# Kernel tuning notes

Hardware: AMD Instinct MI355X
Metric: run time of the kernel (lower is better)

Reference implementation:

```python
import jax, jax.numpy as jnp
import numpy as np

HIDDEN = 4096
INTER = 11008
BATCH, SEQ = 2, 2048


def setup_inputs() -> dict:
    key = jax.random.key(0)
    ks = jax.random.split(key, 7)
    s_h = 1.0 / np.sqrt(HIDDEN)   # nn.Linear default init bound fan_in=HIDDEN
    s_i = 1.0 / np.sqrt(INTER)    # fan_in=INTER for down_proj
    return {
        "hidden_states": jax.random.normal(ks[0], (BATCH, SEQ, HIDDEN), dtype=jnp.float32),
        "w_gate": jax.random.uniform(ks[1], (INTER, HIDDEN), jnp.float32, -s_h, s_h),
        "b_gate": jax.random.uniform(ks[2], (INTER,), jnp.float32, -s_h, s_h),
        "w_up": jax.random.uniform(ks[3], (INTER, HIDDEN), jnp.float32, -s_h, s_h),
        "b_up": jax.random.uniform(ks[4], (INTER,), jnp.float32, -s_h, s_h),
        "w_down": jax.random.uniform(ks[5], (HIDDEN, INTER), jnp.float32, -s_i, s_i),
        "b_down": jax.random.uniform(ks[6], (HIDDEN,), jnp.float32, -s_i, s_i),
    }


def reference(hidden_states, w_gate, b_gate, w_up, b_up, w_down, b_down):
    # SwiGLU MLP: down( silu(gate(x)) * up(x) )
    gate = jax.nn.silu(jnp.einsum("bsh,ih->bsi", hidden_states, w_gate) + b_gate)
    up = jnp.einsum("bsh,ih->bsi", hidden_states, w_up) + b_up
    return jnp.einsum("bsi,hi->bsh", gate * up, w_down) + b_down
```

## Files before the change

kernel.cpp:

```cpp
#include <hip/hip_runtime.h>
#include <hip/hip_bf16.h>


#define M_TOK 4096
#define HID   4096
#define INT_  11008

typedef __attribute__((ext_vector_type(8))) short bf16x8;
typedef __attribute__((ext_vector_type(4))) float f32x4;

__device__ __forceinline__ unsigned short f2bf(float f) {
    union { float f; unsigned int u; } a; a.f = f;
    unsigned int u = a.u;
    u += 0x7fff + ((u >> 16) & 1);
    return (unsigned short)(u >> 16);
}

__device__ __forceinline__ float bf2f(unsigned short h) {
    union { unsigned int u; float f; } a; a.u = ((unsigned int)h) << 16;
    return a.f;
}

__global__ void cvt_f32_bf16(const float* __restrict__ in, unsigned short* __restrict__ out, int n4) {
    int stride = gridDim.x * blockDim.x;
    for (int i = blockIdx.x * blockDim.x + threadIdx.x; i < n4; i += stride) {
        float4 v = ((const float4*)in)[i];
        ushort4 o;
        o.x = f2bf(v.x); o.y = f2bf(v.y); o.z = f2bf(v.z); o.w = f2bf(v.w);
        ((ushort4*)out)[i] = o;
    }
}

#define GLL(gsrc, ldst) \
    __builtin_amdgcn_global_load_lds( \
        (__attribute__((address_space(1))) void*)(gsrc), \
        (__attribute__((address_space(3))) void*)(ldst), 16, 0, 0)

#define VMC(n) asm volatile("s_waitcnt vmcnt(" #n ")" ::: "memory")
#define BARR __builtin_amdgcn_s_barrier()
#define PIN  __builtin_amdgcn_sched_barrier(0)

__global__ __launch_bounds__(512, 2)
void gemm_gu(const unsigned short* __restrict__ A,
             const unsigned short* __restrict__ Wg,
             const unsigned short* __restrict__ Wu,
             const float* __restrict__ bg,
             const float* __restrict__ bu,
             unsigned short* __restrict__ T,
             int M, int NI, int K) {
    __shared__ unsigned short lds[2 * 32768];

    const int tid  = threadIdx.x;
    const int lane = tid & 63;
    const int w    = tid >> 6;
    const int wm   = w >> 2;
    const int wn   = w & 3;

    const int ntn = NI >> 7;
    const int chunk = gridDim.x >> 3;
    const int sw = (blockIdx.x & 7) * chunk + (blockIdx.x >> 3);
    const int bm = sw / ntn, bn = sw % ntn;

    const unsigned short* Ag  = A  + (size_t)(bm * 256) * K;
    const unsigned short* Bgg = Wg + (size_t)(bn * 128) * K;
    const unsigned short* Bug = Wu + (size_t)(bn * 128) * K;

    int offA[2][2], offBW[2];
#pragma unroll
    for (int i = 0; i < 2; ++i) {
        int sig = i * 512 + tid;
        int r   = sig >> 3;
        int s   = (sig & 7) ^ (r & 7);
#pragma unroll
        for (int h = 0; h < 2; ++h) {
            int grow = ((r >> 6) * 2 + h) * 64 + (r & 63);
            offA[h][i] = grow * K + s * 8;
        }
        offBW[i] = r * K + s * 8;
    }

    const int rl = lane & 15;
    const int kg = lane >> 4;
    const int x  = rl & 7;
    const int aRow  = (wm * 64 + rl) * 64;
    const int bGoff = 16384 + (wn * 32 + rl) * 64;
    const int bUoff = 24576 + (wn * 32 + rl) * 64;
    int slt[2];
#pragma unroll
    for (int ks = 0; ks < 2; ++ks) slt[ks] = ((ks * 4 + kg) ^ x) * 8;

    f32x4 accg[2][8], accu[2][8];
#pragma unroll
    for (int q = 0; q < 2; ++q)
#pragma unroll
        for (int f = 0; f < 8; ++f) {
            accg[q][f] = (f32x4){0.f, 0.f, 0.f, 0.f};
            accu[q][f] = (f32x4){0.f, 0.f, 0.f, 0.f};
        }

    const int NT = K >> 6;

#define STAGE_A(H, DST, SRC) \
    GLL((SRC) + offA[H][0], (DST) + (H) * 8192 + tid * 8); \
    GLL((SRC) + offA[H][1], (DST) + (H) * 8192 + 4096 + tid * 8)
#define STAGE_W(BASE, DST, SRC) \
    GLL((SRC) + offBW[0], (DST) + (BASE) + tid * 8); \
    GLL((SRC) + offBW[1], (DST) + (BASE) + 4096 + tid * 8)

#define RD_A(BUF, QM, DST) \
    { _Pragma("unroll") for (int ks = 0; ks < 2; ++ks) \
      _Pragma("unroll") for (int fm = 0; fm < 4; ++fm) \
        DST[ks * 4 + fm] = *(const bf16x8*)((BUF) + (QM) * 8192 + aRow + fm * 1024 + slt[ks]); }
#define RD_W(BUF, ROFF, DST) \
    { _Pragma("unroll") for (int ks = 0; ks < 2; ++ks) \
      _Pragma("unroll") for (int fn = 0; fn < 2; ++fn) \
        DST[ks * 2 + fn] = *(const bf16x8*)((BUF) + (ROFF) + fn * 1024 + slt[ks]); }
#define Q16(ACC, QM, AF, BF) \
    { _Pragma("unroll") for (int ks = 0; ks < 2; ++ks) \
      _Pragma("unroll") for (int fm = 0; fm < 4; ++fm) \
      _Pragma("unroll") for (int fn = 0; fn < 2; ++fn) \
        ACC[QM][fm * 2 + fn] = __builtin_amdgcn_mfma_f32_16x16x32_bf16( \
            AF[ks * 4 + fm], BF[ks * 2 + fn], ACC[QM][fm * 2 + fn], 0, 0, 0); }

    bf16x8 A0f[8], A1f[8], Bgf[4], Buf_[4];

    STAGE_A(0, lds, Ag);
    STAGE_W(16384, lds, Bgg);
    STAGE_W(24576, lds, Bug);
    STAGE_A(1, lds, Ag);
    VMC(2);
    BARR; PIN;

    for (int t = 0; t < NT; ++t) {
        const unsigned short* bc = lds + (t & 1) * 32768;
        unsigned short* sb = lds + ((t + 1) & 1) * 32768;
        const int ts = (t + 1 < NT) ? (t + 1) : (NT - 1);
        const unsigned short* sA = Ag + (size_t)ts * 64;
        const unsigned short* sG = Bgg + (size_t)ts * 64;
        const unsigned short* sU = Bug + (size_t)ts * 64;

        RD_A(bc, 0, A0f);
        RD_W(bc, bGoff, Bgf);
        STAGE_A(0, sb, sA);
        Q16(accg, 0, A0f, Bgf);
        RD_W(bc, bUoff, Buf_);
        STAGE_W(16384, sb, sG);
        Q16(accu, 0, A0f, Buf_);
        STAGE_W(24576, sb, sU);
        VMC(6);
        BARR; PIN;

        RD_A(bc, 1, A1f);
        STAGE_A(1, sb, sA);
        Q16(accg, 1, A1f, Bgf);
        Q16(accu, 1, A1f, Buf_);
        VMC(2);
        BARR; PIN;
    }
#undef RD_A
#undef RD_W
#undef Q16
#undef STAGE_A
#undef STAGE_W

    const int rbase = bm * 256 + wm * 128 + (lane >> 4) * 4;
    const int cbase = bn * 128 + wn * 32 + (lane & 15);
#pragma unroll
    for (int qm = 0; qm < 2; ++qm)
#pragma unroll
        for (int fn = 0; fn < 2; ++fn) {
            const int col = cbase + fn * 16;
            const float bgv = bg[col];
            const float buv = bu[col];
#pragma unroll
            for (int fm = 0; fm < 4; ++fm) {
                const int rb = rbase + qm * 64 + fm * 16;
#pragma unroll
                for (int j = 0; j < 4; ++j) {
                    float g = accg[qm][fm * 2 + fn][j] + bgv;
                    float u = accu[qm][fm * 2 + fn][j] + buv;
                    float s = g / (1.f + __expf(-g)) * u;
                    T[(size_t)(rb + j) * (size_t)INT_ + col] = f2bf(s);
                }
            }
        }
}

__global__ __launch_bounds__(512, 2)
void gemm_dn(const unsigned short* __restrict__ A,
             const unsigned short* __restrict__ B,
             const float* __restrict__ bias,
             float* __restrict__ C,
             int M, int N, int K) {
    __shared__ unsigned short lds[2 * 32768];

    const int tid  = threadIdx.x;
    const int lane = tid & 63;
    const int w    = tid >> 6;
    const int wm   = w >> 2;
    const int wn   = w & 3;

    const int ntn = N >> 8;
    const int chunk = gridDim.x >> 3;
    const int sw = (blockIdx.x & 7) * chunk + (blockIdx.x >> 3);
    const int bm = sw / ntn, bn = sw % ntn;

    const unsigned short* Ag = A + (size_t)(bm * 256) * K;
    const unsigned short* Bg = B + (size_t)(bn * 256) * K;

    int offA[2][2], offB[2][2];
#pragma unroll
    for (int h = 0; h < 2; ++h)
#pragma unroll
        for (int i = 0; i < 2; ++i) {
            int sig = i * 512 + tid;
            int r   = sig >> 3;
            int s   = (sig & 7) ^ (r & 7);
            int grow = ((r >> 6) * 2 + h) * 64 + (r & 63);
            int gcol = ((r >> 5) * 2 + h) * 32 + (r & 31);
            offA[h][i] = grow * K + s * 8;
            offB[h][i] = gcol * K + s * 8;
        }

    const int rl = lane & 15;
    const int kg = lane >> 4;
    const int x  = rl & 7;
    const int aRow = (wm * 64 + rl) * 64;
    const int bRow = 16384 + (wn * 32 + rl) * 64;
    int slt[2];
#pragma unroll
    for (int ks = 0; ks < 2; ++ks) slt[ks] = ((ks * 4 + kg) ^ x) * 8;

    f32x4 acc[2][2][8];
#pragma unroll
    for (int qm = 0; qm < 2; ++qm)
#pragma unroll
        for (int qn = 0; qn < 2; ++qn)
#pragma unroll
            for (int f = 0; f < 8; ++f)
                acc[qm][qn][f] = (f32x4){0.f, 0.f, 0.f, 0.f};

    const int NT = K >> 6;

#define STAGE_A(H, DST, SRC) \
    GLL((SRC) + offA[H][0], (DST) + (H) * 8192 + tid * 8); \
    GLL((SRC) + offA[H][1], (DST) + (H) * 8192 + 4096 + tid * 8)
#define STAGE_B(H, DST, SRC) \
    GLL((SRC) + offB[H][0], (DST) + 16384 + (H) * 8192 + tid * 8); \
    GLL((SRC) + offB[H][1], (DST) + 16384 + (H) * 8192 + 4096 + tid * 8)
#define RD_A(BUF, QM, DST) \
    { _Pragma("unroll") for (int ks = 0; ks < 2; ++ks) \
      _Pragma("unroll") for (int fm = 0; fm < 4; ++fm) \
        DST[ks * 4 + fm] = *(const bf16x8*)((BUF) + (QM) * 8192 + aRow + fm * 1024 + slt[ks]); }
#define RD_B(BUF, QN, DST) \
    { _Pragma("unroll") for (int ks = 0; ks < 2; ++ks) \
      _Pragma("unroll") for (int fn = 0; fn < 2; ++fn) \
        DST[ks * 2 + fn] = *(const bf16x8*)((BUF) + (QN) * 8192 + bRow + fn * 1024 + slt[ks]); }
#define Q16(QM, QN, AF, BF) \
    { _Pragma("unroll") for (int ks = 0; ks < 2; ++ks) \
      _Pragma("unroll") for (int fm = 0; fm < 4; ++fm) \
      _Pragma("unroll") for (int fn = 0; fn < 2; ++fn) \
        acc[QM][QN][fm * 2 + fn] = __builtin_amdgcn_mfma_f32_16x16x32_bf16( \
            AF[ks * 4 + fm], BF[ks * 2 + fn], acc[QM][QN][fm * 2 + fn], 0, 0, 0); }

    bf16x8 A0f[8], A1f[8], B0f[4], B1f[4];

    STAGE_A(0, lds, Ag); STAGE_B(0, lds, Bg); STAGE_B(1, lds, Bg); STAGE_A(1, lds, Ag);
    VMC(2);
    BARR; PIN;

    for (int t = 0; t < NT; ++t) {
        const unsigned short* bc = lds + (t & 1) * 32768;
        unsigned short* sb = lds + ((t + 1) & 1) * 32768;
        const int ts = (t + 1 < NT) ? (t + 1) : (NT - 1);
        const unsigned short* sAt = Ag + (size_t)ts * 64;
        const unsigned short* sBt = Bg + (size_t)ts * 64;

        RD_A(bc, 0, A0f);
        RD_B(bc, 0, B0f);
        STAGE_A(0, sb, sAt);
        Q16(0, 0, A0f, B0f);
        RD_B(bc, 1, B1f);
        STAGE_B(0, sb, sBt);
        Q16(0, 1, A0f, B1f);
        STAGE_B(1, sb, sBt);
        VMC(6);
        BARR; PIN;

        RD_A(bc, 1, A1f);
        STAGE_A(1, sb, sAt);
        Q16(1, 1, A1f, B1f);
        Q16(1, 0, A1f, B0f);
        VMC(2);
        BARR; PIN;
    }
#undef RD_A
#undef RD_B
#undef Q16
#undef STAGE_A
#undef STAGE_B

    const int rbase = bm * 256 + wm * 128 + (lane >> 4) * 4;
    const int cbase = bn * 256 + wn * 64 + (lane & 15);
#pragma unroll
    for (int qm = 0; qm < 2; ++qm)
#pragma unroll
        for (int qn = 0; qn < 2; ++qn)
#pragma unroll
            for (int fn = 0; fn < 2; ++fn) {
                const int col = cbase + qn * 32 + fn * 16;
                const float bv = bias[col];
#pragma unroll
                for (int fm = 0; fm < 4; ++fm) {
                    const int rb = rbase + qm * 64 + fm * 16;
#pragma unroll
                    for (int j = 0; j < 4; ++j)
                        C[(size_t)(rb + j) * (size_t)N + col] = acc[qm][qn][fm * 2 + fn][j] + bv;
                }
            }
}

extern "C" void kernel_launch(void* const* d_in, const int* in_sizes, int n_in,
                              void* d_out, int out_size, void* d_ws, size_t ws_size,
                              hipStream_t stream) {
    const float* x  = (const float*)d_in[0];
    const float* wg = (const float*)d_in[1];
    const float* bg = (const float*)d_in[2];
    const float* wu = (const float*)d_in[3];
    const float* bu = (const float*)d_in[4];
    const float* wd = (const float*)d_in[5];
    const float* bd = (const float*)d_in[6];

    const size_t NX = (size_t)M_TOK * HID;
    const size_t NW = (size_t)INT_ * HID;

    unsigned short* ws = (unsigned short*)d_ws;
    unsigned short* Xb = ws;
    unsigned short* S1 = Xb + NX;
    unsigned short* S2 = S1 + NW;
    unsigned short* S3 = S2 + NW;

    dim3 blk512(512);
    dim3 blk256(256);
    const int CG = 2048;

    cvt_f32_bf16<<<CG, blk256, 0, stream>>>(x,  Xb, (int)(NX / 4));
    cvt_f32_bf16<<<CG, blk256, 0, stream>>>(wg, S1, (int)(NW / 4));
    cvt_f32_bf16<<<CG, blk256, 0, stream>>>(wu, S2, (int)(NW / 4));
    gemm_gu<<<dim3(16 * 86), blk512, 0, stream>>>(Xb, S1, S2, bg, bu, S3,
                                                  M_TOK, INT_, HID);
    cvt_f32_bf16<<<CG, blk256, 0, stream>>>(wd, S1, (int)(NW / 4));
    gemm_dn<<<dim3(16 * 16), blk512, 0, stream>>>(S3, S1, bd, (float*)d_out,
                                                  M_TOK, HID, INT_);
}
```

Baseline: 1.013 ms.

## Fuse fp32-to-bf16 weight conversion into GEMM tile staging via registers

Removes the three separate weight conversion kernels and has both GEMMs read fp32 weights directly from global memory into registers, convert them to bf16 and write them into LDS. This avoids writing and re-reading bf16 copies of roughly 135M weight elements per call. In exchange, every M-tile block re-reads the weights at twice the byte width, uses more registers and VGPR-to-LDS writes instead of direct global-to-LDS loads, and adds extra waitcnt synchronisation to the pipeline.

```diff
diff --git a/kernel.cpp b/kernel.cpp
--- a/kernel.cpp
+++ b/kernel.cpp
@@ -16,9 +16,13 @@
     return (unsigned short)(u >> 16);
 }
 
-__device__ __forceinline__ float bf2f(unsigned short h) {
-    union { unsigned int u; float f; } a; a.u = ((unsigned int)h) << 16;
-    return a.f;
+__device__ __forceinline__ bf16x8 pack8(f32x4 a, f32x4 b) {
+    bf16x8 r;
+    r[0] = (short)f2bf(a[0]); r[1] = (short)f2bf(a[1]);
+    r[2] = (short)f2bf(a[2]); r[3] = (short)f2bf(a[3]);
+    r[4] = (short)f2bf(b[0]); r[5] = (short)f2bf(b[1]);
+    r[6] = (short)f2bf(b[2]); r[7] = (short)f2bf(b[3]);
+    return r;
 }
 
 __global__ void cvt_f32_bf16(const float* __restrict__ in, unsigned short* __restrict__ out, int n4) {
@@ -37,13 +41,24 @@
         (__attribute__((address_space(3))) void*)(ldst), 16, 0, 0)
 
 #define VMC(n) asm volatile("s_waitcnt vmcnt(" #n ")" ::: "memory")
+#define LGKM0  asm volatile("s_waitcnt lgkmcnt(0)" ::: "memory")
 #define BARR __builtin_amdgcn_s_barrier()
 #define PIN  __builtin_amdgcn_sched_barrier(0)
 
+#define WLOAD(DST, SRC, O0, O1) \
+    DST[0] = *(const f32x4*)((SRC) + (O0));      \
+    DST[1] = *(const f32x4*)((SRC) + (O0) + 4);  \
+    DST[2] = *(const f32x4*)((SRC) + (O1));      \
+    DST[3] = *(const f32x4*)((SRC) + (O1) + 4);
+
+#define WWRITE(BASE, SBUF, REGS) \
+    *(bf16x8*)((SBUF) + (BASE) + tid * 8)        = pack8(REGS[0], REGS[1]); \
+    *(bf16x8*)((SBUF) + (BASE) + 4096 + tid * 8) = pack8(REGS[2], REGS[3]);
+
 __global__ __launch_bounds__(512, 2)
 void gemm_gu(const unsigned short* __restrict__ A,
-             const unsigned short* __restrict__ Wg,
-             const unsigned short* __restrict__ Wu,
+             const float* __restrict__ Wg,
+             const float* __restrict__ Wu,
              const float* __restrict__ bg,
              const float* __restrict__ bu,
              unsigned short* __restrict__ T,
@@ -62,10 +77,10 @@
     const int bm = sw / ntn, bn = sw % ntn;
 
     const unsigned short* Ag  = A  + (size_t)(bm * 256) * K;
-    const unsigned short* Bgg = Wg + (size_t)(bn * 128) * K;
-    const unsigned short* Bug = Wu + (size_t)(bn * 128) * K;
-
-    int offA[2][2], offBW[2];
+    const float* Wgg = Wg + (size_t)(bn * 128) * K;
+    const float* Wug = Wu + (size_t)(bn * 128) * K;
+
+    int offA[2][2], offW[2];
 #pragma unroll
     for (int i = 0; i < 2; ++i) {
         int sig = i * 512 + tid;
@@ -76,7 +91,7 @@
             int grow = ((r >> 6) * 2 + h) * 64 + (r & 63);
             offA[h][i] = grow * K + s * 8;
         }
-        offBW[i] = r * K + s * 8;
+        offW[i] = r * K + s * 8;
     }
 
     const int rl = lane & 15;
@@ -103,10 +118,6 @@
 #define STAGE_A(H, DST, SRC) \
     GLL((SRC) + offA[H][0], (DST) + (H) * 8192 + tid * 8); \
     GLL((SRC) + offA[H][1], (DST) + (H) * 8192 + 4096 + tid * 8)
-#define STAGE_W(BASE, DST, SRC) \
-    GLL((SRC) + offBW[0], (DST) + (BASE) + tid * 8); \
-    GLL((SRC) + offBW[1], (DST) + (BASE) + 4096 + tid * 8)
-
 #define RD_A(BUF, QM, DST) \
     { _Pragma("unroll") for (int ks = 0; ks < 2; ++ks) \
       _Pragma("unroll") for (int fm = 0; fm < 4; ++fm) \
@@ -123,12 +134,17 @@
             AF[ks * 4 + fm], BF[ks * 2 + fn], ACC[QM][fm * 2 + fn], 0, 0, 0); }
 
     bf16x8 A0f[8], A1f[8], Bgf[4], Buf_[4];
-
+    f32x4 wgr[4], wur[4];
+
+    WLOAD(wgr, Wgg, offW[0], offW[1]);
+    WLOAD(wur, Wug, offW[0], offW[1]);
+    PIN;
     STAGE_A(0, lds, Ag);
-    STAGE_W(16384, lds, Bgg);
-    STAGE_W(24576, lds, Bug);
     STAGE_A(1, lds, Ag);
-    VMC(2);
+    WWRITE(16384, lds, wgr);
+    WWRITE(24576, lds, wur);
+    VMC(0);
+    LGKM0;
     BARR; PIN;
 
     for (int t = 0; t < NT; ++t) {
@@ -136,32 +152,36 @@
         unsigned short* sb = lds + ((t + 1) & 1) * 32768;
         const int ts = (t + 1 < NT) ? (t + 1) : (NT - 1);
         const unsigned short* sA = Ag + (size_t)ts * 64;
-        const unsigned short* sG = Bgg + (size_t)ts * 64;
-        const unsigned short* sU = Bug + (size_t)ts * 64;
+        const float* sG = Wgg + (size_t)ts * 64;
+        const float* sU = Wug + (size_t)ts * 64;
 
         RD_A(bc, 0, A0f);
         RD_W(bc, bGoff, Bgf);
+        RD_W(bc, bUoff, Buf_);
+        WLOAD(wgr, sG, offW[0], offW[1]);
+        WLOAD(wur, sU, offW[0], offW[1]);
+        PIN;
         STAGE_A(0, sb, sA);
         Q16(accg, 0, A0f, Bgf);
-        RD_W(bc, bUoff, Buf_);
-        STAGE_W(16384, sb, sG);
         Q16(accu, 0, A0f, Buf_);
-        STAGE_W(24576, sb, sU);
-        VMC(6);
+        VMC(10);
         BARR; PIN;
 
         RD_A(bc, 1, A1f);
         STAGE_A(1, sb, sA);
         Q16(accg, 1, A1f, Bgf);
         Q16(accu, 1, A1f, Buf_);
+        VMC(4);
+        WWRITE(16384, sb, wgr);
+        WWRITE(24576, sb, wur);
         VMC(2);
+        LGKM0;
         BARR; PIN;
     }
 #undef RD_A
 #undef RD_W
 #undef Q16
 #undef STAGE_A
-#undef STAGE_W
 
     const int rbase = bm * 256 + wm * 128 + (lane >> 4) * 4;
     const int cbase = bn * 128 + wn * 32 + (lane & 15);
@@ -188,7 +208,7 @@
 
 __global__ __launch_bounds__(512, 2)
 void gemm_dn(const unsigned short* __restrict__ A,
-             const unsigned short* __restrict__ B,
+             const float* __restrict__ B,
              const float* __restrict__ bias,
              float* __restrict__ C,
              int M, int N, int K) {
@@ -206,9 +226,9 @@
     const int bm = sw / ntn, bn = sw % ntn;
 
     const unsigned short* Ag = A + (size_t)(bm * 256) * K;
-    const unsigned short* Bg = B + (size_t)(bn * 256) * K;
-
-    int offA[2][2], offB[2][2];
+    const float* Bg = B + (size_t)(bn * 256) * K;
+
+    int offA[2][2], offW[2][2];
 #pragma unroll
     for (int h = 0; h < 2; ++h)
 #pragma unroll
@@ -219,7 +239,7 @@
             int grow = ((r >> 6) * 2 + h) * 64 + (r & 63);
             int gcol = ((r >> 5) * 2 + h) * 32 + (r & 31);
             offA[h][i] = grow * K + s * 8;
-            offB[h][i] = gcol * K + s * 8;
+            offW[h][i] = gcol * K + s * 8;
         }
 
     const int rl = lane & 15;
@@ -245,9 +265,6 @@
 #define STAGE_A(H, DST, SRC) \
     GLL((SRC) + offA[H][0], (DST) + (H) * 8192 + tid * 8); \
     GLL((SRC) + offA[H][1], (DST) + (H) * 8192 + 4096 + tid * 8)
-#define STAGE_B(H, DST, SRC) \
-    GLL((SRC) + offB[H][0], (DST) + 16384 + (H) * 8192 + tid * 8); \
-    GLL((SRC) + offB[H][1], (DST) + 16384 + (H) * 8192 + 4096 + tid * 8)
 #define RD_A(BUF, QM, DST) \
     { _Pragma("unroll") for (int ks = 0; ks < 2; ++ks) \
       _Pragma("unroll") for (int fm = 0; fm < 4; ++fm) \
@@ -264,9 +281,17 @@
             AF[ks * 4 + fm], BF[ks * 2 + fn], acc[QM][QN][fm * 2 + fn], 0, 0, 0); }
 
     bf16x8 A0f[8], A1f[8], B0f[4], B1f[4];
-
-    STAGE_A(0, lds, Ag); STAGE_B(0, lds, Bg); STAGE_B(1, lds, Bg); STAGE_A(1, lds, Ag);
-    VMC(2);
+    f32x4 w0[4], w1[4];
+
+    WLOAD(w0, Bg, offW[0][0], offW[0][1]);
+    WLOAD(w1, Bg, offW[1][0], offW[1][1]);
+    PIN;
+    STAGE_A(0, lds, Ag);
+    STAGE_A(1, lds, Ag);
+    WWRITE(16384, lds, w0);
+    WWRITE(24576, lds, w1);
+    VMC(0);
+    LGKM0;
     BARR; PIN;
 
     for (int t = 0; t < NT; ++t) {
@@ -274,31 +299,35 @@
         unsigned short* sb = lds + ((t + 1) & 1) * 32768;
         const int ts = (t + 1 < NT) ? (t + 1) : (NT - 1);
         const unsigned short* sAt = Ag + (size_t)ts * 64;
-        const unsigned short* sBt = Bg + (size_t)ts * 64;
+        const float* sBt = Bg + (size_t)ts * 64;
 
         RD_A(bc, 0, A0f);
         RD_B(bc, 0, B0f);
+        WLOAD(w0, sBt, offW[0][0], offW[0][1]);
+        WLOAD(w1, sBt, offW[1][0], offW[1][1]);
+        PIN;
         STAGE_A(0, sb, sAt);
         Q16(0, 0, A0f, B0f);
         RD_B(bc, 1, B1f);
-        STAGE_B(0, sb, sBt);
         Q16(0, 1, A0f, B1f);
-        STAGE_B(1, sb, sBt);
-        VMC(6);
+        VMC(10);
         BARR; PIN;
 
         RD_A(bc, 1, A1f);
         STAGE_A(1, sb, sAt);
         Q16(1, 1, A1f, B1f);
         Q16(1, 0, A1f, B0f);
+        VMC(4);
+        WWRITE(16384, sb, w0);
+        WWRITE(24576, sb, w1);
         VMC(2);
+        LGKM0;
         BARR; PIN;
     }
 #undef RD_A
 #undef RD_B
 #undef Q16
 #undef STAGE_A
-#undef STAGE_B
 
     const int rbase = bm * 256 + wm * 128 + (lane >> 4) * 4;
     const int cbase = bn * 256 + wn * 64 + (lane & 15);
@@ -332,24 +361,18 @@
     const float* bd = (const float*)d_in[6];
 
     const size_t NX = (size_t)M_TOK * HID;
-    const size_t NW = (size_t)INT_ * HID;
+    const size_t NW = (size_t)M_TOK * INT_;
 
     unsigned short* ws = (unsigned short*)d_ws;
     unsigned short* Xb = ws;
-    unsigned short* S1 = Xb + NX;
-    unsigned short* S2 = S1 + NW;
-    unsigned short* S3 = S2 + NW;
+    unsigned short* Tt = Xb + NX;
 
     dim3 blk512(512);
     dim3 blk256(256);
-    const int CG = 2048;
-
-    cvt_f32_bf16<<<CG, blk256, 0, stream>>>(x,  Xb, (int)(NX / 4));
-    cvt_f32_bf16<<<CG, blk256, 0, stream>>>(wg, S1, (int)(NW / 4));
-    cvt_f32_bf16<<<CG, blk256, 0, stream>>>(wu, S2, (int)(NW / 4));
-    gemm_gu<<<dim3(16 * 86), blk512, 0, stream>>>(Xb, S1, S2, bg, bu, S3,
+
+    cvt_f32_bf16<<<2048, blk256, 0, stream>>>(x, Xb, (int)(NX / 4));
+    gemm_gu<<<dim3(16 * 86), blk512, 0, stream>>>(Xb, wg, wu, bg, bu, Tt,
                                                   M_TOK, INT_, HID);
-    cvt_f32_bf16<<<CG, blk256, 0, stream>>>(wd, S1, (int)(NW / 4));
-    gemm_dn<<<dim3(16 * 16), blk512, 0, stream>>>(S3, S1, bd, (float*)d_out,
+    gemm_dn<<<dim3(16 * 16), blk512, 0, stream>>>(Tt, wd, bd, (float*)d_out,
                                                   M_TOK, HID, INT_);
 }
```

After: 1.557 ms. 1.54x slower.

## Merge input conversions into one kernel and overlap w_down conversion with gate/up GEMM

Applied to the files above, without the earlier changes.

The three fp32-to-bf16 conversion launches for x, w_gate and w_up become one kernel. The w_down conversion now runs as 128 extra blocks appended to the gate/up GEMM grid, writing into a fourth workspace buffer, so it can overlap with the GEMM tail instead of being a separate serialized launch. This path needs a larger workspace and falls back to the old sequence when the workspace is too small. The extra blocks compete with GEMM blocks for CUs and bandwidth.

```diff
diff --git a/kernel.cpp b/kernel.cpp
--- a/kernel.cpp
+++ b/kernel.cpp
@@ -5,6 +5,8 @@
 #define M_TOK 4096
 #define HID   4096
 #define INT_  11008
+#define NGU   1376
+#define NCVT  128
 
 typedef __attribute__((ext_vector_type(8))) short bf16x8;
 typedef __attribute__((ext_vector_type(4))) float f32x4;
@@ -16,9 +18,22 @@
     return (unsigned short)(u >> 16);
 }
 
-__device__ __forceinline__ float bf2f(unsigned short h) {
-    union { unsigned int u; float f; } a; a.u = ((unsigned int)h) << 16;
-    return a.f;
+__global__ void cvt3(const float* __restrict__ x,  unsigned short* __restrict__ xb,
+                     const float* __restrict__ wg, unsigned short* __restrict__ s1,
+                     const float* __restrict__ wu, unsigned short* __restrict__ s2,
+                     int n4x, int n4w) {
+    const int total = n4x + 2 * n4w;
+    const int stride = gridDim.x * blockDim.x;
+    for (int i = blockIdx.x * blockDim.x + threadIdx.x; i < total; i += stride) {
+        const float* src; unsigned short* dst; int j;
+        if (i < n4x)            { j = i;             src = x;  dst = xb; }
+        else if (i < n4x + n4w) { j = i - n4x;       src = wg; dst = s1; }
+        else                    { j = i - n4x - n4w; src = wu; dst = s2; }
+        float4 v = ((const float4*)src)[j];
+        ushort4 o;
+        o.x = f2bf(v.x); o.y = f2bf(v.y); o.z = f2bf(v.z); o.w = f2bf(v.w);
+        ((ushort4*)dst)[j] = o;
+    }
 }
 
 __global__ void cvt_f32_bf16(const float* __restrict__ in, unsigned short* __restrict__ out, int n4) {
@@ -47,17 +62,36 @@
              const float* __restrict__ bg,
              const float* __restrict__ bu,
              unsigned short* __restrict__ T,
+             const float* __restrict__ wdSrc,
+             unsigned short* __restrict__ wdDst,
              int M, int NI, int K) {
     __shared__ unsigned short lds[2 * 32768];
 
     const int tid  = threadIdx.x;
+
+    if (blockIdx.x >= NGU) {
+        const int c = blockIdx.x - NGU;
+        const size_t base = (size_t)c * 88064;
+        const float4* src = (const float4*)wdSrc + base;
+        ushort4* dst = (ushort4*)wdDst + base;
+#pragma unroll 4
+        for (int it = 0; it < 172; ++it) {
+            const int u = it * 512 + tid;
+            float4 v = src[u];
+            ushort4 o;
+            o.x = f2bf(v.x); o.y = f2bf(v.y); o.z = f2bf(v.z); o.w = f2bf(v.w);
+            dst[u] = o;
+        }
+        return;
+    }
+
     const int lane = tid & 63;
     const int w    = tid >> 6;
     const int wm   = w >> 2;
     const int wn   = w & 3;
 
     const int ntn = NI >> 7;
-    const int chunk = gridDim.x >> 3;
+    const int chunk = NGU >> 3;
     const int sw = (blockIdx.x & 7) * chunk + (blockIdx.x >> 3);
     const int bm = sw / ntn, bn = sw % ntn;
 
@@ -339,17 +373,28 @@
     unsigned short* S1 = Xb + NX;
     unsigned short* S2 = S1 + NW;
     unsigned short* S3 = S2 + NW;
+    unsigned short* S4 = S3 + NW;
+
+    const bool fused = ws_size >= (NX + 4 * NW) * 2;
 
     dim3 blk512(512);
     dim3 blk256(256);
-    const int CG = 2048;
-
-    cvt_f32_bf16<<<CG, blk256, 0, stream>>>(x,  Xb, (int)(NX / 4));
-    cvt_f32_bf16<<<CG, blk256, 0, stream>>>(wg, S1, (int)(NW / 4));
-    cvt_f32_bf16<<<CG, blk256, 0, stream>>>(wu, S2, (int)(NW / 4));
-    gemm_gu<<<dim3(16 * 86), blk512, 0, stream>>>(Xb, S1, S2, bg, bu, S3,
+
+    cvt3<<<2048, blk256, 0, stream>>>(x, Xb, wg, S1, wu, S2,
+                                      (int)(NX / 4), (int)(NW / 4));
+
+    if (fused) {
+        gemm_gu<<<dim3(NGU + NCVT), blk512, 0, stream>>>(Xb, S1, S2, bg, bu, S3,
+                                                         wd, S4, M_TOK, INT_, HID);
+        gemm_dn<<<dim3(16 * 16), blk512, 0, stream>>>(S3, S4, bd, (float*)d_out,
+                                                      M_TOK, HID, INT_);
+    } else {
+        gemm_gu<<<dim3(NGU), blk512, 0, stream>>>(Xb, S1, S2, bg, bu, S3,
+                                                  (const float*)nullptr,
+                                                  (unsigned short*)nullptr,
                                                   M_TOK, INT_, HID);
-    cvt_f32_bf16<<<CG, blk256, 0, stream>>>(wd, S1, (int)(NW / 4));
-    gemm_dn<<<dim3(16 * 16), blk512, 0, stream>>>(S3, S1, bd, (float*)d_out,
-                                                  M_TOK, HID, INT_);
-}
+        cvt_f32_bf16<<<2048, blk256, 0, stream>>>(wd, S1, (int)(NW / 4));
+        gemm_dn<<<dim3(16 * 16), blk512, 0, stream>>>(S3, S1, bd, (float*)d_out,
+                                                      M_TOK, HID, INT_);
+    }
+}
```

After: 997.1 us. No clear change (-1.6%).
